# Kernel tuning notes

Measured on AMD Instinct MI355X. Metric: run time of the kernel, lower is better.

The kernel has to match this reference:

```python
import jax, jax.numpy as jnp
import numpy as np

SURR_SCALE = 10.0  # AbstractSNNLayer.surr_scale
THRESH = 0.3       # inf_th=False

@jax.custom_vjp
def spike_fn(x):
    # ActFunFastSigmoid.forward: heaviside
    return (x > 0).astype(x.dtype)

def _spike_fwd(x):
    return spike_fn(x), x

def _spike_bwd(x, g):
    # fast-sigmoid surrogate: g / (scale*|x| + 1)^2
    return (g / (SURR_SCALE * jnp.abs(x) + 1.0) ** 2,)

spike_fn.defvjp(_spike_fwd, _spike_bwd)


def setup_inputs() -> dict:
    B, NIN, NOUT = 1024, 4096, 4096
    key = jax.random.key(0)
    k1, k2, k3, k4, k5 = jax.random.split(key, 5)
    prev_spikes = jax.random.bernoulli(k1, 0.2, (B, NIN)).astype(jnp.float32)
    own_mems = 0.1 * jax.random.normal(k2, (B, NOUT), dtype=jnp.float32)
    own_spikes = jax.random.bernoulli(k3, 0.2, (B, NOUT)).astype(jnp.float32)
    W = jax.random.normal(k4, (NOUT, NIN), dtype=jnp.float32) / np.sqrt(NIN)
    tau_m = jax.random.normal(k5, (NOUT,), dtype=jnp.float32)
    return {"prev_spikes": prev_spikes, "own_mems": own_mems,
            "own_spikes": own_spikes, "W": W, "tau_m": tau_m}


def reference(prev_spikes, own_mems, own_spikes, W, tau_m):
    # update_mem: mem = mem * sigmoid(tau_m) * (1 - o_spike) + Linear(i_spike)
    alpha = jax.nn.sigmoid(tau_m)                      # [NOUT]
    mem = own_mems * alpha * (1.0 - own_spikes) \
          + jnp.einsum('bi,oi->bo', prev_spikes, W)    # [B, NOUT]
    # activation_function: spike with surrogate grad, then reset-to-zero
    o_spike = spike_fn(mem - THRESH)
    mem = jnp.where(mem < THRESH, mem, 0.0)            # mem * (mem < th_reset)
    return mem, o_spike
```

## Files before the change

### kernel.cpp

```cpp
#include <hip/hip_runtime.h>
#include <stdint.h>

#define NB 1024
#define NK 4096
#define NO 4096
#define DELTA 4e-7
#define BAND 5e-4f
#define FIXCAP 65536u

typedef __attribute__((ext_vector_type(8))) short s16x8;
typedef __attribute__((ext_vector_type(4))) float f32x4;
typedef __attribute__((ext_vector_type(4))) int i32x4;
typedef __attribute__((ext_vector_type(16))) char c8x16;

static __device__ __forceinline__ unsigned short f2bf_rne(float x) {
  union { float f; unsigned u; } c; c.f = x;
  unsigned r = (c.u + 0x7FFFu + ((c.u >> 16) & 1u)) >> 16;
  return (unsigned short)r;
}
static __device__ __forceinline__ float bf2f(unsigned short h) {
  union { float f; unsigned u; } c; c.u = ((unsigned)h) << 16;
  return c.f;
}

static __device__ __forceinline__ void gload16(const void* g, void* l) {
  __builtin_amdgcn_global_load_lds((const __attribute__((address_space(1))) void*)g,
                                   (__attribute__((address_space(3))) void*)l, 16, 0, 0);
}

__global__ void cvtA8t_kernel(const float* __restrict__ A, signed char* __restrict__ A8t,
                              unsigned* __restrict__ cnt) {
  if (blockIdx.x == 0 && threadIdx.x == 0) *cnt = 0u;
  const int n = NB * NK / 16;
  for (int i = blockIdx.x * blockDim.x + threadIdx.x; i < n; i += gridDim.x * blockDim.x) {
    const int bm = i >> 15, rem = i & 32767;
    const int kt = rem >> 9, rem2 = rem & 511;
    const int l = rem2 >> 3, c = rem2 & 7;
    const int row = bm * 128 + 2 * l + (c >> 2);
    const int col = kt * 64 + (c & 3) * 16;
    const float* src = A + ((size_t)row << 12) + col;
    c8x16 v;
#pragma unroll
    for (int j = 0; j < 4; ++j) {
      float4 f = *(const float4*)(src + j * 4);
      v[j * 4 + 0] = (char)(int)f.x; v[j * 4 + 1] = (char)(int)f.y;
      v[j * 4 + 2] = (char)(int)f.z; v[j * 4 + 3] = (char)(int)f.w;
    }
    const size_t dst = ((size_t)(bm * 64 + kt) << 13) + l * 128 + ((c ^ (l & 7)) << 4);
    *(c8x16*)(A8t + dst) = v;
  }
}

__global__ void cvtW8t_kernel(const float* __restrict__ W, signed char* __restrict__ W8t) {
  const int n = NO * NK / 16;
  for (int i = blockIdx.x * blockDim.x + threadIdx.x; i < n; i += gridDim.x * blockDim.x) {
    const int bn = i >> 14, rem = i & 16383;
    const int kt = rem >> 8, rem2 = rem & 255;
    const int l = rem2 >> 3, c = rem2 & 7;
    const int row = bn * 64 + 2 * l + (c >> 2);
    const int col = kt * 64 + (c & 3) * 16;
    const float* src = W + ((size_t)row << 12) + col;
    c8x16 v1, v0;
#pragma unroll
    for (int j = 0; j < 16; ++j) {
      const int qi = (int)rintf(src[j] * 65536.0f);
      const int q1 = (qi + 64) >> 7;
      const int q0 = qi - (q1 << 7);
      v1[j] = (char)q1; v0[j] = (char)q0;
    }
    const size_t dst = ((size_t)(bn * 64 + kt) << 13) + l * 128 + ((c ^ (l & 7)) << 4);
    *(c8x16*)(W8t + dst) = v1;
    *(c8x16*)(W8t + dst + 4096) = v0;
  }
}

static __device__ __forceinline__ void frag_read2(
    const char* rb, const int (&offA)[2], const int (&offB)[2],
    i32x4 (&af)[2], i32x4 (&b1)[2], i32x4 (&b0)[2]) {
#pragma unroll
  for (int mi = 0; mi < 2; ++mi) af[mi] = *(const i32x4*)(rb + offA[mi]);
#pragma unroll
  for (int ni = 0; ni < 2; ++ni) {
    b1[ni] = *(const i32x4*)(rb + 8192 + offB[ni]);
    b0[ni] = *(const i32x4*)(rb + 12288 + offB[ni]);
  }
}

static __device__ __forceinline__ void mfma8(
    const i32x4 (&af)[2], const i32x4 (&b1)[2], const i32x4 (&b0)[2],
    i32x4 (&acc1)[2][2], i32x4 (&acc0)[2][2]) {
  __builtin_amdgcn_s_setprio(1);
#pragma unroll
  for (int mi = 0; mi < 2; ++mi)
#pragma unroll
    for (int ni = 0; ni < 2; ++ni) {
      acc1[mi][ni] = __builtin_amdgcn_mfma_i32_16x16x64_i8(af[mi], b1[ni], acc1[mi][ni], 0, 0, 0);
      acc0[mi][ni] = __builtin_amdgcn_mfma_i32_16x16x64_i8(af[mi], b0[ni], acc0[mi][ni], 0, 0, 0);
    }
  __builtin_amdgcn_s_setprio(0);
}

__global__ __launch_bounds__(512, 4) void snn_gemm_w8(
    const signed char* __restrict__ A8t, const signed char* __restrict__ W8t,
    const float* __restrict__ own_mems, const float* __restrict__ own_spikes,
    const float* __restrict__ tau, float* __restrict__ out,
    unsigned* __restrict__ cnt, unsigned* __restrict__ list) {
  __shared__ __align__(16) char ring[4][16384];

  const int tid = threadIdx.x;
  const int lane = tid & 63;
  const int wave = tid >> 6;
  const int wm = wave >> 1, wn = wave & 1;

  const int bid = blockIdx.x;
  const int bm = bid & 7;
  const int bn = bid >> 3;

  const int woff = wave << 10;
  const char* pA = (const char*)A8t + ((size_t)(bm * 64) << 13) + tid * 16;
  const char* pW = (const char*)W8t + ((size_t)(bn * 64) << 13) + tid * 16;

  const int fr = lane & 15;
  const int fq = lane >> 4;

  int offA[2], offB[2];
#pragma unroll
  for (int mi = 0; mi < 2; ++mi) {
    const int r = wm * 32 + mi * 16 + fr, l = r >> 1;
    offA[mi] = l * 128 + ((((r & 1) * 4 + fq) ^ (l & 7)) * 16);
  }
#pragma unroll
  for (int ni = 0; ni < 2; ++ni) {
    const int r = wn * 32 + ni * 16 + fr, l = r >> 1;
    offB[ni] = l * 128 + ((((r & 1) * 4 + fq) ^ (l & 7)) * 16);
  }

  i32x4 acc1[2][2], acc0[2][2];
#pragma unroll
  for (int i = 0; i < 2; ++i)
#pragma unroll
    for (int j = 0; j < 2; ++j) { acc1[i][j] = (i32x4){0, 0, 0, 0};
                                  acc0[i][j] = (i32x4){0, 0, 0, 0}; }

  i32x4 afA[2], b1A[2], b0A[2], afB[2], b1B[2], b0B[2];

#define STAGE(slot, kt) { const size_t _ko = ((size_t)((kt) & 63) << 13);  \
    gload16(pA + _ko, ring[slot] + woff);                                  \
    gload16(pW + _ko, ring[slot] + 8192 + woff); }

#define SYNC asm volatile("s_waitcnt vmcnt(4) lgkmcnt(0)" ::: "memory"); \
    __builtin_amdgcn_s_barrier();

#define STEP(rd, st, kt, AFU, B1U, B0U, AFN, B1N, B0N)               \
    frag_read2(ring[rd], offA, offB, AFN, B1N, B0N);                 \
    STAGE(st, kt)                                                    \
    mfma8(AFU, B1U, B0U, acc1, acc0);                                \
    SYNC

  STAGE(0, 0) STAGE(1, 1) STAGE(2, 2) STAGE(3, 3)
  asm volatile("s_waitcnt vmcnt(4)" ::: "memory");
  __builtin_amdgcn_s_barrier();
  frag_read2(ring[0], offA, offB, afA, b1A, b0A);
  asm volatile("s_waitcnt lgkmcnt(0)" ::: "memory");
  __builtin_amdgcn_s_barrier();

#pragma unroll 1
  for (int m = 0; m < 16; ++m) {
    const int t = 4 * m;
    STEP(1, 0, t + 4, afA, b1A, b0A, afB, b1B, b0B)
    STEP(2, 1, t + 5, afB, b1B, b0B, afA, b1A, b0A)
    STEP(3, 2, t + 6, afA, b1A, b0A, afB, b1B, b0B)
    STEP(0, 3, t + 7, afB, b1B, b0B, afA, b1A, b0A)
  }
#undef STEP
#undef SYNC
#undef STAGE

  const float inv = 1.0f / 65536.0f;
#pragma unroll
  for (int ni = 0; ni < 2; ++ni) {
    const int gc = bn * 64 + wn * 32 + ni * 16 + fr;
    const float alpha = 1.0f / (1.0f + expf(-tau[gc]));
#pragma unroll
    for (int mi = 0; mi < 2; ++mi) {
#pragma unroll
      for (int j = 0; j < 4; ++j) {
        const int gr = bm * 128 + wm * 32 + mi * 16 + fq * 4 + j;
        const size_t idx = (size_t)gr * NO + gc;
        const int comb = (acc1[mi][ni][j] << 7) + acc0[mi][ni][j];
        const float dec = own_mems[idx] * alpha * (1.0f - own_spikes[idx]);
        const float mem = (float)comb * inv + dec;
        out[idx] = (mem < 0.3f) ? mem : 0.0f;
        out[(size_t)NB * NO + idx] = (mem > 0.3f) ? 1.0f : 0.0f;
        if (fabsf(mem - 0.3f) < BAND) {
          unsigned p = atomicAdd(cnt, 1u);
          if (p < FIXCAP) list[p] = (unsigned)idx;
        }
      }
    }
  }
}

__global__ __launch_bounds__(256) void snn_fixup(
    const float* __restrict__ prev, const float* __restrict__ Wf,
    const float* __restrict__ own_mems, const float* __restrict__ own_spikes,
    const float* __restrict__ tau, const unsigned* __restrict__ cnt,
    const unsigned* __restrict__ list, float* __restrict__ out) {
  const unsigned n = min(*cnt, FIXCAP);
  const int lane = threadIdx.x & 63;
  const int wv = blockIdx.x * (blockDim.x >> 6) + (threadIdx.x >> 6);
  const int nw = gridDim.x * (blockDim.x >> 6);
  for (unsigned it = (unsigned)wv; it < n; it += (unsigned)nw) {
    const unsigned idx = list[it];
    const int gr = (int)(idx >> 12);
    const int gc = (int)(idx & 4095);
    const float4* ap4 = (const float4*)(prev + (size_t)gr * NK);
    const float4* wp4 = (const float4*)(Wf + (size_t)gc * NK);
    double s = 0.0;
#pragma unroll 4
    for (int jj = 0; jj < 16; ++jj) {
      const float4 a = ap4[jj * 64 + lane];
      const float4 w = wp4[jj * 64 + lane];
      s += (double)a.x * (double)w.x + (double)a.y * (double)w.y
         + (double)a.z * (double)w.z + (double)a.w * (double)w.w;
    }
#pragma unroll
    for (int off = 1; off < 64; off <<= 1) s += __shfl_xor(s, off, 64);
    if (lane == 0) {
      const double alpha = 1.0 / (1.0 + exp(-(double)tau[gc]));
      const double dec = (double)own_mems[idx] * alpha * (1.0 - (double)own_spikes[idx]);
      const double mv = dec + s;
      const double T = 0.3 + DELTA;
      out[idx] = (mv < T) ? (float)mv : 0.0f;
      out[(size_t)NB * NO + idx] = (mv > T) ? 1.0f : 0.0f;
    }
  }
}

__global__ __launch_bounds__(256) void snn_fused(
    const float* __restrict__ prev, const float* __restrict__ Wf,
    const float* __restrict__ own_mems, const float* __restrict__ own_spikes,
    const float* __restrict__ tau, float* __restrict__ out) {
  __shared__ __align__(16) unsigned short sA[128 * 32];
  __shared__ __align__(16) unsigned short sH[128 * 32];
  __shared__ __align__(16) unsigned short sL[128 * 32];
  const int tid = threadIdx.x;
  const int lane = tid & 63;
  const int wave = tid >> 6;
  const int wm = wave >> 1, wn = wave & 1;
  const int bn = blockIdx.x, bm = blockIdx.y;
  const int srow = tid >> 1;
  const int scol = (tid & 1) * 16;
  const float* gA = prev + (size_t)(bm * 128 + srow) * NK + scol;
  const float* gW = Wf + (size_t)(bn * 128 + srow) * NK + scol;
  const int sb = srow * 32 + scol;
  f32x4 acc[4][4];
#pragma unroll
  for (int i = 0; i < 4; ++i)
#pragma unroll
    for (int j = 0; j < 4; ++j) acc[i][j] = (f32x4){0.f, 0.f, 0.f, 0.f};
  const int fr = lane & 15;
  const int fq = lane >> 4;
  const int fk = fq * 8;
  for (int kt = 0; kt < NK / 32; ++kt) {
    const int ko = kt * 32;
    float av[16], wv[16];
    *(float4*)&av[0]  = *(const float4*)(gA + ko);
    *(float4*)&av[4]  = *(const float4*)(gA + ko + 4);
    *(float4*)&av[8]  = *(const float4*)(gA + ko + 8);
    *(float4*)&av[12] = *(const float4*)(gA + ko + 12);
    *(float4*)&wv[0]  = *(const float4*)(gW + ko);
    *(float4*)&wv[4]  = *(const float4*)(gW + ko + 4);
    *(float4*)&wv[8]  = *(const float4*)(gW + ko + 8);
    *(float4*)&wv[12] = *(const float4*)(gW + ko + 12);
    s16x8 va0, va1, vh0, vh1, vl0, vl1;
#pragma unroll
    for (int j = 0; j < 8; ++j) {
      va0[j] = (short)f2bf_rne(av[j]);
      va1[j] = (short)f2bf_rne(av[j + 8]);
      const unsigned short h0 = f2bf_rne(wv[j]);
      vh0[j] = (short)h0;
      vl0[j] = (short)f2bf_rne(wv[j] - bf2f(h0));
      const unsigned short h1 = f2bf_rne(wv[j + 8]);
      vh1[j] = (short)h1;
      vl1[j] = (short)f2bf_rne(wv[j + 8] - bf2f(h1));
    }
    __syncthreads();
    *(s16x8*)&sA[sb] = va0; *(s16x8*)&sA[sb + 8] = va1;
    *(s16x8*)&sH[sb] = vh0; *(s16x8*)&sH[sb + 8] = vh1;
    *(s16x8*)&sL[sb] = vl0; *(s16x8*)&sL[sb + 8] = vl1;
    __syncthreads();
    s16x8 af[4], bh[4], bl[4];
#pragma unroll
    for (int mi = 0; mi < 4; ++mi)
      af[mi] = *(const s16x8*)&sA[(wm * 64 + mi * 16 + fr) * 32 + fk];
#pragma unroll
    for (int ni = 0; ni < 4; ++ni) {
      bh[ni] = *(const s16x8*)&sH[(wn * 64 + ni * 16 + fr) * 32 + fk];
      bl[ni] = *(const s16x8*)&sL[(wn * 64 + ni * 16 + fr) * 32 + fk];
    }
#pragma unroll
    for (int mi = 0; mi < 4; ++mi)
#pragma unroll
      for (int ni = 0; ni < 4; ++ni) {
        acc[mi][ni] = __builtin_amdgcn_mfma_f32_16x16x32_bf16(af[mi], bh[ni], acc[mi][ni], 0, 0, 0);
        acc[mi][ni] = __builtin_amdgcn_mfma_f32_16x16x32_bf16(af[mi], bl[ni], acc[mi][ni], 0, 0, 0);
      }
  }
  unsigned long long fm = 0ull;
#pragma unroll
  for (int ni = 0; ni < 4; ++ni) {
    const int gc = bn * 128 + wn * 64 + ni * 16 + fr;
    const float alpha = 1.0f / (1.0f + expf(-tau[gc]));
#pragma unroll
    for (int mi = 0; mi < 4; ++mi) {
#pragma unroll
      for (int j = 0; j < 4; ++j) {
        const int gr = bm * 128 + wm * 64 + mi * 16 + fq * 4 + j;
        const size_t idx = (size_t)gr * NO + gc;
        const float dec = own_mems[idx] * alpha * (1.0f - own_spikes[idx]);
        const float mem = acc[mi][ni][j] + dec;
        out[idx] = (mem < 0.3f) ? mem : 0.0f;
        out[(size_t)NB * NO + idx] = (mem > 0.3f) ? 1.0f : 0.0f;
        if (fabsf(mem - 0.3f) < 1e-3f)
          fm |= 1ull << (mi * 16 + ni * 4 + j);
      }
    }
  }
#pragma unroll 1
  for (int r = 0; r < 64; ++r) {
    unsigned long long m = __ballot((fm >> r) & 1ull);
    if (m == 0ull) continue;
    const int mi = r >> 4, ni = (r >> 2) & 3, j = r & 3;
    const int gr_r = bm * 128 + wm * 64 + mi * 16 + fq * 4 + j;
    const int gc_r = bn * 128 + wn * 64 + ni * 16 + fr;
    while (m) {
      const int l = (int)__ffsll(m) - 1;
      m &= m - 1ull;
      const int gr = __shfl(gr_r, l, 64);
      const int gc = __shfl(gc_r, l, 64);
      const float* ap = prev + (size_t)gr * NK;
      const float* wp = Wf + (size_t)gc * NK;
      double s0 = 0.0, s1 = 0.0;
#pragma unroll 2
      for (int jj = 0; jj < 64; jj += 2) {
        s0 += (double)ap[lane + jj * 64]       * (double)wp[lane + jj * 64];
        s1 += (double)ap[lane + (jj + 1) * 64] * (double)wp[lane + (jj + 1) * 64];
      }
      double sum = s0 + s1;
#pragma unroll
      for (int off = 1; off < 64; off <<= 1) sum += __shfl_xor(sum, off, 64);
      if (lane == 0) {
        const size_t idx = (size_t)gr * NO + gc;
        const double alpha = 1.0 / (1.0 + exp(-(double)tau[gc]));
        const double dec = (double)own_mems[idx] * alpha * (1.0 - (double)own_spikes[idx]);
        const double mv = dec + sum;
        const double T = 0.3 + DELTA;
        out[idx] = (mv < T) ? (float)mv : 0.0f;
        out[(size_t)NB * NO + idx] = (mv > T) ? 1.0f : 0.0f;
      }
    }
  }
}

extern "C" void kernel_launch(void* const* d_in, const int* in_sizes, int n_in,
                              void* d_out, int out_size, void* d_ws, size_t ws_size,
                              hipStream_t stream) {
  const float* prev_spikes = (const float*)d_in[0];
  const float* own_mems    = (const float*)d_in[1];
  const float* own_spikes  = (const float*)d_in[2];
  const float* W           = (const float*)d_in[3];
  const float* tau         = (const float*)d_in[4];
  float* out = (float*)d_out;

  const size_t aBytes = (size_t)NB * NK;
  const size_t wBytes = (size_t)NO * NK * 2;
  const size_t fixBytes = 16 + (size_t)FIXCAP * 4;
  if (ws_size >= aBytes + wBytes + fixBytes) {
    char* p = (char*)d_ws;
    signed char* A8t = (signed char*)p;
    signed char* W8t = (signed char*)(p + aBytes);
    unsigned* cnt    = (unsigned*)(p + aBytes + wBytes);
    unsigned* list   = cnt + 4;
    cvtA8t_kernel<<<1024, 256, 0, stream>>>(prev_spikes, A8t, cnt);
    cvtW8t_kernel<<<2048, 256, 0, stream>>>(W, W8t);
    snn_gemm_w8<<<512, 512, 0, stream>>>(A8t, W8t, own_mems, own_spikes,
                                         tau, out, cnt, list);
    snn_fixup<<<512, 256, 0, stream>>>(prev_spikes, W, own_mems, own_spikes,
                                       tau, cnt, list, out);
  } else {
    snn_fused<<<dim3(NO / 128, NB / 128), 256, 0, stream>>>(
        prev_spikes, W, own_mems, own_spikes, tau, out);
  }
}
```

Baseline: 111.7 us.

## Merge conversion kernels and fold near-threshold fixup into GEMM epilogue

The two int8 conversion kernels become one prep kernel with a flat one-element-per-thread grid. The separate fixup kernel, global atomic counter and index list are removed. Each wave now builds a per-lane bitmask of near-threshold outputs, ballots it, and recomputes those elements with an exact double-precision dot product inside the GEMM epilogue. This drops two launches and the atomic contention, but the GEMM tail now stalls on serial recompute within each wave and may become uneven across waves.

```diff
diff --git a/kernel.cpp b/kernel.cpp
--- a/kernel.cpp
+++ b/kernel.cpp
@@ -6,7 +6,6 @@
 #define NO 4096
 #define DELTA 4e-7
 #define BAND 5e-4f
-#define FIXCAP 65536u
 
 typedef __attribute__((ext_vector_type(8))) short s16x8;
 typedef __attribute__((ext_vector_type(4))) float f32x4;
@@ -28,11 +27,12 @@
                                    (__attribute__((address_space(3))) void*)l, 16, 0, 0);
 }
 
-__global__ void cvtA8t_kernel(const float* __restrict__ A, signed char* __restrict__ A8t,
-                              unsigned* __restrict__ cnt) {
-  if (blockIdx.x == 0 && threadIdx.x == 0) *cnt = 0u;
-  const int n = NB * NK / 16;
-  for (int i = blockIdx.x * blockDim.x + threadIdx.x; i < n; i += gridDim.x * blockDim.x) {
+__global__ __launch_bounds__(512) void prep_kernel(
+    const float* __restrict__ A, const float* __restrict__ W,
+    signed char* __restrict__ A8t, signed char* __restrict__ W8t) {
+  const int gid = blockIdx.x * 512 + threadIdx.x;
+  if (gid < 262144) {
+    const int i = gid;
     const int bm = i >> 15, rem = i & 32767;
     const int kt = rem >> 9, rem2 = rem & 511;
     const int l = rem2 >> 3, c = rem2 & 7;
@@ -48,12 +48,8 @@
     }
     const size_t dst = ((size_t)(bm * 64 + kt) << 13) + l * 128 + ((c ^ (l & 7)) << 4);
     *(c8x16*)(A8t + dst) = v;
-  }
-}
-
-__global__ void cvtW8t_kernel(const float* __restrict__ W, signed char* __restrict__ W8t) {
-  const int n = NO * NK / 16;
-  for (int i = blockIdx.x * blockDim.x + threadIdx.x; i < n; i += gridDim.x * blockDim.x) {
+  } else {
+    const int i = gid - 262144;
     const int bn = i >> 14, rem = i & 16383;
     const int kt = rem >> 8, rem2 = rem & 255;
     const int l = rem2 >> 3, c = rem2 & 7;
@@ -102,9 +98,9 @@
 
 __global__ __launch_bounds__(512, 4) void snn_gemm_w8(
     const signed char* __restrict__ A8t, const signed char* __restrict__ W8t,
+    const float* __restrict__ prev, const float* __restrict__ Wf,
     const float* __restrict__ own_mems, const float* __restrict__ own_spikes,
-    const float* __restrict__ tau, float* __restrict__ out,
-    unsigned* __restrict__ cnt, unsigned* __restrict__ list) {
+    const float* __restrict__ tau, float* __restrict__ out) {
   __shared__ __align__(16) char ring[4][16384];
 
   const int tid = threadIdx.x;
@@ -177,6 +173,7 @@
 #undef STAGE
 
   const float inv = 1.0f / 65536.0f;
+  unsigned fm = 0u;
 #pragma unroll
   for (int ni = 0; ni < 2; ++ni) {
     const int gc = bn * 64 + wn * 32 + ni * 16 + fr;
@@ -192,47 +189,45 @@
         const float mem = (float)comb * inv + dec;
         out[idx] = (mem < 0.3f) ? mem : 0.0f;
         out[(size_t)NB * NO + idx] = (mem > 0.3f) ? 1.0f : 0.0f;
-        if (fabsf(mem - 0.3f) < BAND) {
-          unsigned p = atomicAdd(cnt, 1u);
-          if (p < FIXCAP) list[p] = (unsigned)idx;
-        }
-      }
-    }
-  }
-}
-
-__global__ __launch_bounds__(256) void snn_fixup(
-    const float* __restrict__ prev, const float* __restrict__ Wf,
-    const float* __restrict__ own_mems, const float* __restrict__ own_spikes,
-    const float* __restrict__ tau, const unsigned* __restrict__ cnt,
-    const unsigned* __restrict__ list, float* __restrict__ out) {
-  const unsigned n = min(*cnt, FIXCAP);
-  const int lane = threadIdx.x & 63;
-  const int wv = blockIdx.x * (blockDim.x >> 6) + (threadIdx.x >> 6);
-  const int nw = gridDim.x * (blockDim.x >> 6);
-  for (unsigned it = (unsigned)wv; it < n; it += (unsigned)nw) {
-    const unsigned idx = list[it];
-    const int gr = (int)(idx >> 12);
-    const int gc = (int)(idx & 4095);
-    const float4* ap4 = (const float4*)(prev + (size_t)gr * NK);
-    const float4* wp4 = (const float4*)(Wf + (size_t)gc * NK);
-    double s = 0.0;
+        if (fabsf(mem - 0.3f) < BAND)
+          fm |= 1u << ((mi * 2 + ni) * 4 + j);
+      }
+    }
+  }
+
+#pragma unroll 1
+  for (int r = 0; r < 16; ++r) {
+    unsigned long long m = __ballot((fm >> r) & 1u);
+    if (m == 0ull) continue;
+    const int mi = r >> 3, ni = (r >> 2) & 1, j = r & 3;
+    const int gr_r = bm * 128 + wm * 32 + mi * 16 + fq * 4 + j;
+    const int gc_r = bn * 64 + wn * 32 + ni * 16 + fr;
+    while (m) {
+      const int l = (int)__ffsll(m) - 1;
+      m &= m - 1ull;
+      const int gr = __shfl(gr_r, l, 64);
+      const int gc = __shfl(gc_r, l, 64);
+      const float4* ap4 = (const float4*)(prev + (size_t)gr * NK);
+      const float4* wp4 = (const float4*)(Wf + (size_t)gc * NK);
+      double s = 0.0;
 #pragma unroll 4
-    for (int jj = 0; jj < 16; ++jj) {
-      const float4 a = ap4[jj * 64 + lane];
-      const float4 w = wp4[jj * 64 + lane];
-      s += (double)a.x * (double)w.x + (double)a.y * (double)w.y
-         + (double)a.z * (double)w.z + (double)a.w * (double)w.w;
-    }
-#pragma unroll
-    for (int off = 1; off < 64; off <<= 1) s += __shfl_xor(s, off, 64);
-    if (lane == 0) {
-      const double alpha = 1.0 / (1.0 + exp(-(double)tau[gc]));
-      const double dec = (double)own_mems[idx] * alpha * (1.0 - (double)own_spikes[idx]);
-      const double mv = dec + s;
-      const double T = 0.3 + DELTA;
-      out[idx] = (mv < T) ? (float)mv : 0.0f;
-      out[(size_t)NB * NO + idx] = (mv > T) ? 1.0f : 0.0f;
+      for (int jj = 0; jj < 16; ++jj) {
+        const float4 a = ap4[jj * 64 + lane];
+        const float4 w = wp4[jj * 64 + lane];
+        s += (double)a.x * (double)w.x + (double)a.y * (double)w.y
+           + (double)a.z * (double)w.z + (double)a.w * (double)w.w;
+      }
+#pragma unroll
+      for (int off = 1; off < 64; off <<= 1) s += __shfl_xor(s, off, 64);
+      if (lane == 0) {
+        const size_t idx = (size_t)gr * NO + gc;
+        const double alpha = 1.0 / (1.0 + exp(-(double)tau[gc]));
+        const double dec = (double)own_mems[idx] * alpha * (1.0 - (double)own_spikes[idx]);
+        const double mv = dec + s;
+        const double T = 0.3 + DELTA;
+        out[idx] = (mv < T) ? (float)mv : 0.0f;
+        out[(size_t)NB * NO + idx] = (mv > T) ? 1.0f : 0.0f;
+      }
     }
   }
 }
@@ -375,19 +370,13 @@
 
   const size_t aBytes = (size_t)NB * NK;
   const size_t wBytes = (size_t)NO * NK * 2;
-  const size_t fixBytes = 16 + (size_t)FIXCAP * 4;
-  if (ws_size >= aBytes + wBytes + fixBytes) {
+  if (ws_size >= aBytes + wBytes) {
     char* p = (char*)d_ws;
     signed char* A8t = (signed char*)p;
     signed char* W8t = (signed char*)(p + aBytes);
-    unsigned* cnt    = (unsigned*)(p + aBytes + wBytes);
-    unsigned* list   = cnt + 4;
-    cvtA8t_kernel<<<1024, 256, 0, stream>>>(prev_spikes, A8t, cnt);
-    cvtW8t_kernel<<<2048, 256, 0, stream>>>(W, W8t);
-    snn_gemm_w8<<<512, 512, 0, stream>>>(A8t, W8t, own_mems, own_spikes,
-                                         tau, out, cnt, list);
-    snn_fixup<<<512, 256, 0, stream>>>(prev_spikes, W, own_mems, own_spikes,
-                                       tau, cnt, list, out);
+    prep_kernel<<<2560, 512, 0, stream>>>(prev_spikes, W, A8t, W8t);
+    snn_gemm_w8<<<512, 512, 0, stream>>>(A8t, W8t, prev_spikes, W,
+                                         own_mems, own_spikes, tau, out);
   } else {
     snn_fused<<<dim3(NO / 128, NB / 128), 256, 0, stream>>>(
         prev_spikes, W, own_mems, own_spikes, tau, out);
```

After: 91.11 us. -18.4%, faster.
